# Kernel optimization log

Measured on AMD Instinct MI355X. Metric: run time of the kernel, lower is better.

The kernel has to match this reference:

```python
import jax, jax.numpy as jnp
import numpy as np

NPIX = 196608  # 12 * NSIDE^2, NSIDE=128
B, CIN, COUT, K = 4, 32, 64, 9


def setup_inputs() -> dict:
    key = jax.random.key(0)
    k1, k2, k3 = jax.random.split(key, 3)
    x = jax.random.normal(k1, (B, CIN, NPIX), dtype=jnp.float32)
    # 9-pt HEALPix stencil indices (random in-range stand-in for precomputed neighbours)
    neighbours = jax.random.randint(k2, (K * NPIX,), 0, NPIX, dtype=jnp.int64)
    # kaiming-normal-ish conv weight [out, in, 9]
    W = jax.random.normal(k3, (COUT, CIN, K), dtype=jnp.float32) * np.float32(np.sqrt(2.0 / (CIN * K)))
    b = jnp.zeros((COUT,), dtype=jnp.float32)
    return {"x": x, "neighbours": neighbours, "W": W, "b": b}


def reference(x, neighbours, W, b):
    # Gather the 9 stencil neighbours per pixel: [B, Cin, npix, 9]
    idx = neighbours.reshape(NPIX, K)
    vec = x[:, :, idx]
    # Conv1d(kernel=9, stride=9) == per-pixel matmul over (Cin, 9)
    out = jnp.einsum('bcpk,ock->bop', vec, W) + b[None, :, None]
    return out  # [B, Cout, npix]
```

## Files before the change

### kernel.cpp

```cpp
#include <hip/hip_runtime.h>
#include <hip/hip_bf16.h>

#define NPIX 196608
#define CIN  32
#define COUT 64
#define KNB  9
#define BATCH 4

typedef short short8 __attribute__((ext_vector_type(8)));
typedef float f32x4  __attribute__((ext_vector_type(4)));
typedef unsigned int uint4v __attribute__((ext_vector_type(4)));

static __device__ __forceinline__ unsigned short f2bf(float f) {
    union { float f; unsigned int u; } v; v.f = f;
    unsigned int r = v.u + 0x7FFFu + ((v.u >> 16) & 1u);
    return (unsigned short)(r >> 16);
}

__global__ __launch_bounds__(256) void wpack_kernel(const float* __restrict__ W,
                                                    unsigned short* __restrict__ Wp) {
    int e = blockIdx.x * 256 + threadIdx.x;
    if (e >= 18432) return;
    int j = e & 7;
    int l = (e >> 3) & 63;
    int m = (e >> 9) & 3;
    int k = e >> 11;
    int o = m * 16 + (l & 15);
    int c = ((l >> 4) << 3) + j;
    Wp[e] = f2bf(W[(o * CIN + c) * KNB + k]);
}

__global__ __launch_bounds__(256) void xpose_kernel(const float* __restrict__ x,
                                                    unsigned short* __restrict__ xT) {
    __shared__ unsigned int lds[64][68];
    int t  = threadIdx.x;
    int p0 = blockIdx.x * 64;
    int c2 = t >> 4;
    int pg = (t & 15) * 4;

    #pragma unroll
    for (int b = 0; b < 4; ++b) {
        const float* xr = x + ((size_t)(b * CIN + 2 * c2)) * NPIX + p0 + pg;
        f32x4 lo = __builtin_nontemporal_load((const f32x4*)xr);
        f32x4 hi = __builtin_nontemporal_load((const f32x4*)(xr + NPIX));
        #pragma unroll
        for (int j = 0; j < 4; ++j)
            lds[pg + j][b * 16 + c2] =
                (unsigned int)f2bf(lo[j]) | ((unsigned int)f2bf(hi[j]) << 16);
    }
    __syncthreads();
    unsigned int* dst = (unsigned int*)xT + (size_t)p0 * 64;
    #pragma unroll
    for (int i = 0; i < 4; ++i) {
        int ub = (i * 256 + t) * 4;
        uint4v v = *(const uint4v*)&lds[ub >> 6][ub & 63];
        __builtin_nontemporal_store(v, (uint4v*)(dst + ub));
    }
}

template <bool TR>
__global__ __launch_bounds__(256, 4) void conv_kernel(const unsigned short* __restrict__ xT,
                                                      const float* __restrict__ x,
                                                      const int* __restrict__ nbr,
                                                      const unsigned short* __restrict__ Wp,
                                                      const float* __restrict__ bias,
                                                      float* __restrict__ out) {
    __shared__ int ilds[576];

    int t  = threadIdx.x;
    int p0 = blockIdx.x * 64;

    for (int i = t; i < 576; i += 256) {
        int idx = __builtin_nontemporal_load(&nbr[p0 * KNB + i]);
        ilds[i] = TR ? (idx << 8) : idx;
    }
    __syncthreads();

    int lane = t & 63;
    int w    = t >> 6;
    int r    = lane & 15;
    int q    = lane >> 4;

    f32x4 acc[4][4] = {};

    const char* xb = (const char*)xT + w * 64 + q * 16;
    const unsigned short* wl = Wp + (size_t)lane * 8;

    int prow[4];
    #pragma unroll
    for (int f = 0; f < 4; ++f) prow[f] = (f * 16 + r) * KNB;

    #pragma unroll
    for (int k = 0; k < KNB; ++k) {
        short8 bfrag[4];
        #pragma unroll
        for (int f = 0; f < 4; ++f) {
            int off = ilds[prow[f] + k];
            if (TR) {
                bfrag[f] = *(const short8*)(xb + off);
            } else {
                const float* xc = x + (size_t)(w * CIN + q * 8) * NPIX + off;
                #pragma unroll
                for (int j = 0; j < 8; ++j)
                    bfrag[f][j] = (short)f2bf(xc[(size_t)j * NPIX]);
            }
        }
        short8 afr[4];
        #pragma unroll
        for (int m = 0; m < 4; ++m)
            afr[m] = *(const short8*)(wl + (((k << 2) | m) << 9));
        #pragma unroll
        for (int m = 0; m < 4; ++m)
            #pragma unroll
            for (int f = 0; f < 4; ++f)
                acc[m][f] = __builtin_amdgcn_mfma_f32_16x16x32_bf16(
                                afr[m], bfrag[f], acc[m][f], 0, 0, 0);
    }

    float* ob = out + (size_t)w * COUT * NPIX + p0 + r;
    #pragma unroll
    for (int m = 0; m < 4; ++m) {
        f32x4 bv = *(const f32x4*)(bias + m * 16 + q * 4);
        #pragma unroll
        for (int rr = 0; rr < 4; ++rr) {
            float* orow = ob + (size_t)(m * 16 + q * 4 + rr) * NPIX;
            #pragma unroll
            for (int f = 0; f < 4; ++f)
                __builtin_nontemporal_store(acc[m][f][rr] + bv[rr], orow + f * 16);
        }
    }
}

extern "C" void kernel_launch(void* const* d_in, const int* in_sizes, int n_in,
                              void* d_out, int out_size, void* d_ws, size_t ws_size,
                              hipStream_t stream) {
    const float* x    = (const float*)d_in[0];
    const int*   nbr  = (const int*)d_in[1];
    const float* W    = (const float*)d_in[2];
    const float* bias = (const float*)d_in[3];
    float*       out  = (float*)d_out;

    const size_t wp_bytes = 18432 * sizeof(unsigned short);
    const size_t wp_pad   = (wp_bytes + 255) & ~(size_t)255;
    const size_t xT_bytes = (size_t)BATCH * NPIX * CIN * 2;

    unsigned short* Wp = (unsigned short*)d_ws;
    unsigned short* xT = (unsigned short*)((char*)d_ws + wp_pad);

    bool full = ws_size >= wp_pad + xT_bytes;

    wpack_kernel<<<72, 256, 0, stream>>>(W, Wp);
    if (full) {
        xpose_kernel<<<NPIX / 64, 256, 0, stream>>>(x, xT);
        conv_kernel<true><<<NPIX / 64, 256, 0, stream>>>(xT, x, nbr, Wp, bias, out);
    } else {
        conv_kernel<false><<<NPIX / 64, 256, 0, stream>>>(xT, x, nbr, Wp, bias, out);
    }
}
```

Before: 154.4 us.

## Stage gathered pixel rows through double-buffered LDS and coalesce output stores

The conv kernel now gathers full 256-byte neighbour pixel rows of the transposed bf16 input once per block into a double-buffered LDS tile, prefetching stencil tap k+1 while computing tap k. Before, each wave gathered its own 64-byte slice. The epilogue also goes through LDS so each output row is written with 16-byte vector stores instead of scalar strided stores. The transpose kernel's stores become normal (cached) so the conv kernel's gathers may hit in cache. This adds per-tap barriers and extra LDS footprint, which may reduce occupancy.

```diff
diff --git a/kernel.cpp b/kernel.cpp
--- a/kernel.cpp
+++ b/kernel.cpp
@@ -54,57 +54,62 @@
     for (int i = 0; i < 4; ++i) {
         int ub = (i * 256 + t) * 4;
         uint4v v = *(const uint4v*)&lds[ub >> 6][ub & 63];
-        __builtin_nontemporal_store(v, (uint4v*)(dst + ub));
-    }
-}
-
-template <bool TR>
-__global__ __launch_bounds__(256, 4) void conv_kernel(const unsigned short* __restrict__ xT,
-                                                      const float* __restrict__ x,
+        *(uint4v*)(dst + ub) = v;
+    }
+}
+
+__global__ __launch_bounds__(256, 4) void conv_staged(const unsigned short* __restrict__ xT,
                                                       const int* __restrict__ nbr,
                                                       const unsigned short* __restrict__ Wp,
                                                       const float* __restrict__ bias,
                                                       float* __restrict__ out) {
+    __shared__ union {
+        unsigned short glds[2][64][136];
+        float          elds[4][16][68];
+    } sh;
     __shared__ int ilds[576];
 
     int t  = threadIdx.x;
     int p0 = blockIdx.x * 64;
 
-    for (int i = t; i < 576; i += 256) {
-        int idx = __builtin_nontemporal_load(&nbr[p0 * KNB + i]);
-        ilds[i] = TR ? (idx << 8) : idx;
-    }
+    for (int i = t; i < 576; i += 256)
+        ilds[i] = __builtin_nontemporal_load(&nbr[p0 * KNB + i]) << 8;
     __syncthreads();
 
     int lane = t & 63;
     int w    = t >> 6;
     int r    = lane & 15;
     int q    = lane >> 4;
+    int lu   = lane >> 4;
+    int lb   = (lane & 15) << 4;
+
+    const char* xTc = (const char*)xT;
+    const unsigned short* wl = Wp + (size_t)lane * 8;
 
     f32x4 acc[4][4] = {};
-
-    const char* xb = (const char*)xT + w * 64 + q * 16;
-    const unsigned short* wl = Wp + (size_t)lane * 8;
-
-    int prow[4];
-    #pragma unroll
-    for (int f = 0; f < 4; ++f) prow[f] = (f * 16 + r) * KNB;
-
-    #pragma unroll
+    short8 g[4];
+
+#define GLOAD(kk)                                                          \
+    { _Pragma("unroll") for (int j = 0; j < 4; ++j) {                      \
+        int iu = (w << 4) + (j << 2) + lu;                                 \
+        g[j] = *(const short8*)(xTc + ilds[iu * 9 + (kk)] + lb); } }
+#define GWRITE(bb)                                                         \
+    { _Pragma("unroll") for (int j = 0; j < 4; ++j) {                      \
+        int iu = (w << 4) + (j << 2) + lu;                                 \
+        *(short8*)&sh.glds[bb][iu][(lane & 15) << 3] = g[j]; } }
+
+    GLOAD(0);
+    GWRITE(0);
+    int cur = 0;
+
     for (int k = 0; k < KNB; ++k) {
+        __syncthreads();
+        if (k < KNB - 1) GLOAD(k + 1);
+
         short8 bfrag[4];
         #pragma unroll
-        for (int f = 0; f < 4; ++f) {
-            int off = ilds[prow[f] + k];
-            if (TR) {
-                bfrag[f] = *(const short8*)(xb + off);
-            } else {
-                const float* xc = x + (size_t)(w * CIN + q * 8) * NPIX + off;
-                #pragma unroll
-                for (int j = 0; j < 8; ++j)
-                    bfrag[f][j] = (short)f2bf(xc[(size_t)j * NPIX]);
-            }
-        }
+        for (int f = 0; f < 4; ++f)
+            bfrag[f] = *(const short8*)&sh.glds[cur][f * 16 + r][(w * 4 + q) << 3];
         short8 afr[4];
         #pragma unroll
         for (int m = 0; m < 4; ++m)
@@ -115,18 +120,82 @@
             for (int f = 0; f < 4; ++f)
                 acc[m][f] = __builtin_amdgcn_mfma_f32_16x16x32_bf16(
                                 afr[m], bfrag[f], acc[m][f], 0, 0, 0);
-    }
-
-    float* ob = out + (size_t)w * COUT * NPIX + p0 + r;
+
+        if (k < KNB - 1) { GWRITE(cur ^ 1); cur ^= 1; }
+    }
+    __syncthreads();
+
+    float* ob = out + (size_t)w * COUT * NPIX + p0;
     #pragma unroll
     for (int m = 0; m < 4; ++m) {
         f32x4 bv = *(const f32x4*)(bias + m * 16 + q * 4);
         #pragma unroll
+        for (int f = 0; f < 4; ++f)
+            #pragma unroll
+            for (int rr = 0; rr < 4; ++rr)
+                sh.elds[w][q * 4 + rr][f * 16 + r] = acc[m][f][rr] + bv[rr];
+        #pragma unroll
+        for (int i = 0; i < 4; ++i) {
+            int gidx = i * 64 + lane;
+            int row  = gidx >> 4;
+            int col  = (gidx & 15) * 4;
+            f32x4 v = *(const f32x4*)&sh.elds[w][row][col];
+            __builtin_nontemporal_store(v,
+                (f32x4*)(ob + (size_t)(m * 16 + row) * NPIX + col));
+        }
+    }
+#undef GLOAD
+#undef GWRITE
+}
+
+__global__ __launch_bounds__(256, 4) void conv_fb(const float* __restrict__ x,
+                                                  const int* __restrict__ nbr,
+                                                  const unsigned short* __restrict__ Wp,
+                                                  const float* __restrict__ bias,
+                                                  float* __restrict__ out) {
+    __shared__ int ilds[576];
+    int t  = threadIdx.x;
+    int p0 = blockIdx.x * 64;
+    for (int i = t; i < 576; i += 256)
+        ilds[i] = nbr[p0 * KNB + i];
+    __syncthreads();
+
+    int lane = t & 63, w = t >> 6, r = lane & 15, q = lane >> 4;
+    f32x4 acc[4][4] = {};
+    const unsigned short* wl = Wp + (size_t)lane * 8;
+
+    #pragma unroll 3
+    for (int k = 0; k < KNB; ++k) {
+        short8 bfrag[4];
+        #pragma unroll
+        for (int f = 0; f < 4; ++f) {
+            int off = ilds[(f * 16 + r) * KNB + k];
+            const float* xc = x + (size_t)(w * CIN + q * 8) * NPIX + off;
+            #pragma unroll
+            for (int j = 0; j < 8; ++j)
+                bfrag[f][j] = (short)f2bf(xc[(size_t)j * NPIX]);
+        }
+        short8 afr[4];
+        #pragma unroll
+        for (int m = 0; m < 4; ++m)
+            afr[m] = *(const short8*)(wl + (((k << 2) | m) << 9));
+        #pragma unroll
+        for (int m = 0; m < 4; ++m)
+            #pragma unroll
+            for (int f = 0; f < 4; ++f)
+                acc[m][f] = __builtin_amdgcn_mfma_f32_16x16x32_bf16(
+                                afr[m], bfrag[f], acc[m][f], 0, 0, 0);
+    }
+    float* ob = out + (size_t)w * COUT * NPIX + p0 + r;
+    #pragma unroll
+    for (int m = 0; m < 4; ++m) {
+        f32x4 bv = *(const f32x4*)(bias + m * 16 + q * 4);
+        #pragma unroll
         for (int rr = 0; rr < 4; ++rr) {
             float* orow = ob + (size_t)(m * 16 + q * 4 + rr) * NPIX;
             #pragma unroll
             for (int f = 0; f < 4; ++f)
-                __builtin_nontemporal_store(acc[m][f][rr] + bv[rr], orow + f * 16);
+                orow[f * 16] = acc[m][f][rr] + bv[rr];
         }
     }
 }
@@ -152,8 +221,8 @@
     wpack_kernel<<<72, 256, 0, stream>>>(W, Wp);
     if (full) {
         xpose_kernel<<<NPIX / 64, 256, 0, stream>>>(x, xT);
-        conv_kernel<true><<<NPIX / 64, 256, 0, stream>>>(xT, x, nbr, Wp, bias, out);
+        conv_staged<<<NPIX / 64, 256, 0, stream>>>(xT, nbr, Wp, bias, out);
     } else {
-        conv_kernel<false><<<NPIX / 64, 256, 0, stream>>>(xT, x, nbr, Wp, bias, out);
-    }
-}
+        conv_fb<<<NPIX / 64, 256, 0, stream>>>(x, nbr, Wp, bias, out);
+    }
+}
```

Measured after the change: 150.4 us. -2.6%, faster.
